# Optimization experiments

Hardware: AMD Instinct MI355X
Metric: run time of the kernel (lower is better)

Reference implementation:

```python
import jax, jax.numpy as jnp
import numpy as np

B, T, E, H, L = 16, 1024, 1024, 512, 6
C = 1024  # conv out channels


def _lstm_dir(x_tbi, Wih, Whh, bih, bhh):
    # x_tbi: [T, B, I]; single-direction LSTM, PyTorch gate order (i, f, g, o)
    Bn = x_tbi.shape[1]
    Hh = Whh.shape[1]
    b = bih + bhh
    def step(carry, xt):
        h, c = carry
        g = xt @ Wih.T + h @ Whh.T + b  # [B, 4H]
        i, f, gg, o = jnp.split(g, 4, axis=-1)
        c = jax.nn.sigmoid(f) * c + jax.nn.sigmoid(i) * jnp.tanh(gg)
        h = jax.nn.sigmoid(o) * jnp.tanh(c)
        return (h, c), h
    h0 = jnp.zeros((Bn, Hh), x_tbi.dtype)
    _, hs = jax.lax.scan(step, (h0, h0), x_tbi)
    return hs  # [T, B, H]


def _forward(embeddings, attention_mask, labels, conv_w, conv_b, bn_gamma, bn_beta,
             bn_mean, bn_var, lstm_Wih, lstm_Whh, lstm_bih, lstm_bhh,
             cls_w, cls_b, crf_start, crf_end, crf_trans):
    # Conv1d(E->1024, k=5, pad=2) on [B, C, T]
    x = jax.lax.conv_general_dilated(
        embeddings.astype(jnp.float32).transpose(0, 2, 1), conv_w,
        window_strides=(1,), padding=[(2, 2)],
        dimension_numbers=("NCH", "OIH", "NCH")) + conv_b[None, :, None]
    # BatchNorm1d (eval: running stats) fused + ReLU
    scale = bn_gamma / jnp.sqrt(bn_var + 1e-5)
    x = jax.nn.relu(x * scale[None, :, None] + (bn_beta - bn_mean * scale)[None, :, None])
    # time-major for the LSTM scans: [T, B, 1024]
    x = x.transpose(2, 0, 1)
    for l in range(3):
        fw = _lstm_dir(x, lstm_Wih[l, 0], lstm_Whh[l, 0], lstm_bih[l, 0], lstm_bhh[l, 0])
        bw = _lstm_dir(x[::-1], lstm_Wih[l, 1], lstm_Whh[l, 1], lstm_bih[l, 1], lstm_bhh[l, 1])[::-1]
        x = jnp.concatenate([fw, bw], axis=-1)  # [T, B, 2H]
    logits = x @ cls_w.T + cls_b  # [T, B, L]; dropout is identity in eval
    # CRF negative log-likelihood (torchcrf, batch_first handled by time-major layout)
    mask = (attention_mask.astype(bool) & (labels != -100)).T  # [T, B]
    tags = jnp.where(labels == -100, 0, labels).astype(jnp.int32).T  # [T, B]
    mf = mask.astype(logits.dtype)
    bidx = jnp.arange(logits.shape[1])
    # numerator: score of the given tag sequence
    score0 = crf_start[tags[0]] + logits[0, bidx, tags[0]]
    def num_step(carry, inp):
        score, prev = carry
        et, mt, mtf, tt = inp
        s = crf_trans[prev, tt] + et[bidx, tt]
        return (score + mtf * s, jnp.where(mt, tt, prev)), None
    (num, last), _ = jax.lax.scan(
        num_step, (score0, tags[0]), (logits[1:], mask[1:], mf[1:], tags[1:]))
    num = num + crf_end[last]
    # denominator: forward algorithm (log partition)
    def den_step(alpha, inp):
        et, mt = inp
        nxt = jax.nn.logsumexp(alpha[:, :, None] + crf_trans[None, :, :] + et[:, None, :], axis=1)
        return jnp.where(mt[:, None], nxt, alpha), None
    alpha, _ = jax.lax.scan(den_step, crf_start + logits[0], (logits[1:], mask[1:]))
    den = jax.nn.logsumexp(alpha + crf_end, axis=-1)
    return -(num - den).mean()  # reduction='mean' over batch, negated


def setup_inputs() -> dict:
    key = jax.random.key(0)
    ks = jax.random.split(key, 16)
    p = lambda k, shp: jax.random.normal(k, shp, jnp.float32) * 0.05
    return {
        "embeddings": jax.random.normal(ks[0], (B, T, E), jnp.float32),
        "attention_mask": jnp.ones((B, T), jnp.int32),
        "labels": jax.random.randint(ks[1], (B, T), 0, L, jnp.int32),
        "conv_w": p(ks[2], (C, E, 5)),
        "conv_b": p(ks[3], (C,)),
        "bn_gamma": jnp.ones((C,), jnp.float32),
        "bn_beta": jnp.zeros((C,), jnp.float32),
        "bn_mean": p(ks[4], (C,)),
        "bn_var": jax.random.uniform(ks[5], (C,), jnp.float32, 0.5, 1.5),
        "lstm_Wih": p(ks[6], (3, 2, 4 * H, C)),
        "lstm_Whh": p(ks[7], (3, 2, 4 * H, H)),
        "lstm_bih": p(ks[8], (3, 2, 4 * H)),
        "lstm_bhh": p(ks[9], (3, 2, 4 * H)),
        "cls_w": p(ks[10], (L, 2 * H)),
        "cls_b": p(ks[11], (L,)),
        "crf_start": p(ks[12], (L,)),
        "crf_end": p(ks[13], (L,)),
        "crf_trans": p(ks[14], (L, L)),
    }


def reference(embeddings, attention_mask, labels, conv_w, conv_b, bn_gamma, bn_beta,
              bn_mean, bn_var, lstm_Wih, lstm_Whh, lstm_bih, lstm_bhh,
              cls_w, cls_b, crf_start, crf_end, crf_trans):
    return _forward(embeddings, attention_mask, labels, conv_w, conv_b, bn_gamma,
                    bn_beta, bn_mean, bn_var, lstm_Wih, lstm_Whh, lstm_bih,
                    lstm_bhh, cls_w, cls_b, crf_start, crf_end, crf_trans)
```

## Files before the change

kernel.cpp:

```cpp
#include <hip/hip_runtime.h>


typedef short bf16_t;
typedef __attribute__((ext_vector_type(8))) short bf16x8;
typedef __attribute__((ext_vector_type(4))) float f32x4;

__device__ __forceinline__ bf16_t f2b(float x) {
  unsigned u = __float_as_uint(x);
  unsigned r = (u + 0x7fffu + ((u >> 16) & 1u)) >> 16;
  return (bf16_t)(unsigned short)r;
}
__device__ __forceinline__ float blo(unsigned u) { return __uint_as_float(u << 16); }
__device__ __forceinline__ float bhi(unsigned u) { return __uint_as_float(u & 0xffff0000u); }


__global__ void embed_pad_k(const float* __restrict__ E, bf16_t* __restrict__ P) {
  size_t i4 = ((size_t)blockIdx.x * 256 + threadIdx.x) * 4;
  if (i4 >= 16ul * 1028 * 1024) return;
  int e = (int)(i4 & 1023);
  size_t rest = i4 >> 10;
  int tp = (int)(rest % 1028);
  int b  = (int)(rest / 1028);
  bf16_t o[4];
  if (tp >= 2 && tp < 1026) {
    const float4 v = *(const float4*)(E + (((size_t)b * 1024 + (tp - 2)) * 1024 + e));
    o[0] = f2b(v.x); o[1] = f2b(v.y); o[2] = f2b(v.z); o[3] = f2b(v.w);
  } else {
    o[0] = o[1] = o[2] = o[3] = 0;
  }
  *(uint2*)(P + i4) = *(const uint2*)o;
}

__global__ void convw_cvt_k(const float* __restrict__ S, bf16_t* __restrict__ D) {
  int idx = blockIdx.x * 256 + threadIdx.x;
  if (idx >= 1024 * 1024) return;
  int c = idx >> 10, e = idx & 1023;
  const float* s = S + (size_t)idx * 5;
#pragma unroll
  for (int kk = 0; kk < 5; kk++) D[(size_t)c * 5120 + kk * 1024 + e] = f2b(s[kk]);
}

__global__ void bnfold_k(const float* cb, const float* g, const float* be,
                         const float* mn, const float* vr, float* a, float* dd) {
  int c = blockIdx.x * 256 + threadIdx.x;
  if (c < 1024) {
    float s = g[c] * rsqrtf(vr[c] + 1e-5f);
    a[c] = s;
    dd[c] = (cb[c] - mn[c]) * s + be[c];
  }
}

__global__ void wihcvt_k(const float* __restrict__ S, bf16_t* __restrict__ D) {
  size_t i = ((size_t)blockIdx.x * 256 + threadIdx.x) * 4;
  if (i >= 3ul * 2 * 2048 * 1024) return;
  float4 v = *(const float4*)(S + i);
  bf16_t o[4] = {f2b(v.x), f2b(v.y), f2b(v.z), f2b(v.w)};
  *(uint2*)(D + i) = *(const uint2*)o;
}

__global__ __launch_bounds__(256, 1) void gemm_bt(
    const bf16_t* __restrict__ A, const bf16_t* __restrict__ W,
    const float* __restrict__ bias0, const float* __restrict__ bias1,
    bf16_t* __restrict__ C, int M, int N, int K) {
  const int tid = threadIdx.x;
  const int nb = N >> 7;
  const int m0 = (blockIdx.x / nb) * 128, n0 = (blockIdx.x % nb) * 128;
  __shared__ bf16_t As[128][72];
  __shared__ bf16_t Bs[128][72];
  const int wv = tid >> 6, ln = tid & 63;
  const int wm = (wv >> 1) * 64, wn = (wv & 1) * 64;
  const int lb = ln & 15, lq = ln >> 4;
  f32x4 acc[4][4] = {};
  for (int k0 = 0; k0 < K; k0 += 64) {
    __syncthreads();
#pragma unroll
    for (int i = 0; i < 4; i++) {
      int idx = tid + i * 256, r = idx >> 3, ch = idx & 7;
      *(uint4*)&As[r][ch * 8] = *(const uint4*)(A + (size_t)(m0 + r) * K + k0 + ch * 8);
      *(uint4*)&Bs[r][ch * 8] = *(const uint4*)(W + (size_t)(n0 + r) * K + k0 + ch * 8);
    }
    __syncthreads();
#pragma unroll
    for (int kk = 0; kk < 2; kk++) {
      bf16x8 af[4], bfr[4];
#pragma unroll
      for (int t = 0; t < 4; t++) {
        af[t]  = *(const bf16x8*)&As[wm + t * 16 + lb][kk * 32 + lq * 8];
        bfr[t] = *(const bf16x8*)&Bs[wn + t * 16 + lb][kk * 32 + lq * 8];
      }
#pragma unroll
      for (int mt = 0; mt < 4; mt++)
#pragma unroll
        for (int nt = 0; nt < 4; nt++)
          acc[mt][nt] = __builtin_amdgcn_mfma_f32_16x16x32_bf16(af[mt], bfr[nt], acc[mt][nt], 0, 0, 0);
    }
  }
#pragma unroll
  for (int mt = 0; mt < 4; mt++)
#pragma unroll
    for (int nt = 0; nt < 4; nt++) {
      int col = n0 + wn + nt * 16 + lb;
      float bs = bias0[col] + bias1[col];
#pragma unroll
      for (int r = 0; r < 4; r++) {
        int row = m0 + wm + mt * 16 + lq * 4 + r;
        C[(size_t)row * N + col] = f2b(acc[mt][nt][r] + bs);
      }
    }
}

__global__ __launch_bounds__(256, 1) void conv_gemm(
    const bf16_t* __restrict__ EP, const bf16_t* __restrict__ Wc,
    const float* __restrict__ bn_a, const float* __restrict__ bn_d,
    bf16_t* __restrict__ X) {
  const int tid = threadIdx.x;
  const int m0 = (blockIdx.x >> 3) * 128, n0 = (blockIdx.x & 7) * 128;
  __shared__ bf16_t As[128][72];
  __shared__ bf16_t Bs[128][72];
  const int wv = tid >> 6, ln = tid & 63;
  const int wm = (wv >> 1) * 64, wn = (wv & 1) * 64;
  const int lb = ln & 15, lq = ln >> 4;
  f32x4 acc[4][4] = {};
  for (int kk = 0; kk < 5; kk++) {
    for (int k0 = 0; k0 < 1024; k0 += 64) {
      __syncthreads();
#pragma unroll
      for (int i = 0; i < 4; i++) {
        int idx = tid + i * 256, r = idx >> 3, ch = idx & 7;
        int m = m0 + r;
        const bf16_t* ap = EP + ((size_t)((m & 15) * 1028 + (m >> 4) + kk)) * 1024 + k0 + ch * 8;
        *(uint4*)&As[r][ch * 8] = *(const uint4*)ap;
        *(uint4*)&Bs[r][ch * 8] = *(const uint4*)(Wc + (size_t)(n0 + r) * 5120 + kk * 1024 + k0 + ch * 8);
      }
      __syncthreads();
#pragma unroll
      for (int kq = 0; kq < 2; kq++) {
        bf16x8 af[4], bfr[4];
#pragma unroll
        for (int t = 0; t < 4; t++) {
          af[t]  = *(const bf16x8*)&As[wm + t * 16 + lb][kq * 32 + lq * 8];
          bfr[t] = *(const bf16x8*)&Bs[wn + t * 16 + lb][kq * 32 + lq * 8];
        }
#pragma unroll
        for (int mt = 0; mt < 4; mt++)
#pragma unroll
          for (int nt = 0; nt < 4; nt++)
            acc[mt][nt] = __builtin_amdgcn_mfma_f32_16x16x32_bf16(af[mt], bfr[nt], acc[mt][nt], 0, 0, 0);
      }
    }
  }
#pragma unroll
  for (int mt = 0; mt < 4; mt++)
#pragma unroll
    for (int nt = 0; nt < 4; nt++) {
      int col = n0 + wn + nt * 16 + lb;
      float sa = bn_a[col], sd = bn_d[col];
#pragma unroll
      for (int r = 0; r < 4; r++) {
        int row = m0 + wm + mt * 16 + lq * 4 + r;
        float v = fmaxf(acc[mt][nt][r] * sa + sd, 0.f);
        X[(size_t)row * 1024 + col] = f2b(v);
      }
    }
}

__global__ __launch_bounds__(256, 1) void rec_kernel(
    const float* __restrict__ Whh,
    const bf16_t* __restrict__ gfw,
    const bf16_t* __restrict__ gbw,
    bf16_t* __restrict__ xout,
    bf16_t* __restrict__ hst,
    float* __restrict__ cst,
    unsigned* __restrict__ bar,
    int t0f, int t0b, int nsteps) {
  const int tid = threadIdx.x;
  const int d  = blockIdx.x >> 5;
  const int j0 = (blockIdx.x & 31) << 4;
  const int wv = tid >> 6;
  const int ln = tid & 63;
  const int lb = ln & 15;
  const int lq = ln >> 4;

  __shared__ bf16_t Hb[16][520];
  __shared__ float  Ex[4][16][17];

  bf16x8 afrag[16];
  {
    const float* wrow = Whh + ((size_t)(d * 2048 + wv * 512 + j0 + lb)) * 512;
#pragma unroll
    for (int kk = 0; kk < 16; kk++) {
      const float* wp = wrow + kk * 32 + lq * 8;
      float4 va = *(const float4*)wp;
      float4 vb = *(const float4*)(wp + 4);
      bf16x8 fr;
      fr[0] = f2b(va.x); fr[1] = f2b(va.y); fr[2] = f2b(va.z); fr[3] = f2b(va.w);
      fr[4] = f2b(vb.x); fr[5] = f2b(vb.y); fr[6] = f2b(vb.z); fr[7] = f2b(vb.w);
      afrag[kk] = fr;
    }
  }
  const int cb = tid >> 4;
  const int cj = tid & 15;
  float creg = cst[((size_t)d * 16 + cb) * 512 + j0 + cj];
  const bf16_t* gates = (d == 0) ? gfw : gbw;

  unsigned g0, g1;
  {
    const int trow = (d == 0) ? 0 : (nsteps - 1);
    const unsigned* gp = (const unsigned*)(gates + ((size_t)trow * 16 + lb) * 2048 + wv * 512 + j0 + lq * 4);
    g0 = gp[0]; g1 = gp[1];
  }

  for (int s = 0; s < nsteps; s++) {
    const int rb = (s & 1) ^ 1, wb = s & 1;
    if (s > 0) {
      if (tid == 0) {
        unsigned target = (unsigned)(64 * s);
        while (__hip_atomic_load(bar, __ATOMIC_RELAXED, __HIP_MEMORY_SCOPE_AGENT) < target)
          __builtin_amdgcn_s_sleep(1);
      }
      __syncthreads();
    }
    {
      const unsigned long long* hsrc =
          (const unsigned long long*)(hst + ((size_t)rb * 2 + d) * 16 * 512);
      unsigned long long v[8];
#pragma unroll
      for (int i = 0; i < 8; i++)
        v[i] = __hip_atomic_load(hsrc + tid + i * 256, __ATOMIC_RELAXED, __HIP_MEMORY_SCOPE_AGENT);
#pragma unroll
      for (int i = 0; i < 8; i++) {
        int idx = tid + i * 256;
        *(unsigned long long*)&Hb[idx >> 7][(idx & 127) * 4] = v[i];
      }
    }
    __syncthreads();
    const int t = (d == 0) ? (t0f + s) : (t0b + nsteps - 1 - s);
    f32x4 acc;
    acc[0] = blo(g0); acc[1] = bhi(g0); acc[2] = blo(g1); acc[3] = bhi(g1);
#pragma unroll
    for (int kk = 0; kk < 16; kk++) {
      bf16x8 bfr = *(const bf16x8*)&Hb[lb][kk * 32 + lq * 8];
      acc = __builtin_amdgcn_mfma_f32_16x16x32_bf16(afrag[kk], bfr, acc, 0, 0, 0);
    }
    if (s + 1 < nsteps) {
      const int trn = (d == 0) ? (s + 1) : (nsteps - 2 - s);
      const unsigned* gpn = (const unsigned*)(gates + ((size_t)trn * 16 + lb) * 2048 + wv * 512 + j0 + lq * 4);
      g0 = gpn[0]; g1 = gpn[1];
    }
#pragma unroll
    for (int r = 0; r < 4; r++) Ex[wv][lq * 4 + r][lb] = acc[r];
    __syncthreads();
    float gi = Ex[0][cj][cb], gf = Ex[1][cj][cb], gg = Ex[2][cj][cb], go = Ex[3][cj][cb];
    float si = 1.f / (1.f + expf(-gi));
    float sf = 1.f / (1.f + expf(-gf));
    float so = 1.f / (1.f + expf(-go));
    creg = sf * creg + si * tanhf(gg);
    float h = so * tanhf(creg);
    bf16_t hb = f2b(h);
    {
      int hi = __shfl_down((int)(unsigned)(unsigned short)hb, 1, 64);
      if ((cj & 1) == 0) {
        unsigned val = (unsigned)(unsigned short)hb | ((unsigned)hi << 16);
        unsigned* hp = (unsigned*)(hst + (((size_t)wb * 2 + d) * 16 + cb) * 512 + j0 + cj);
        __hip_atomic_store(hp, val, __ATOMIC_RELAXED, __HIP_MEMORY_SCOPE_AGENT);
      }
    }
    xout[((size_t)t * 16 + cb) * 1024 + d * 512 + j0 + cj] = hb;
    asm volatile("s_waitcnt vmcnt(0)" ::: "memory");
    __syncthreads();
    if (tid == 0)
      __hip_atomic_fetch_add(bar, 1u, __ATOMIC_RELAXED, __HIP_MEMORY_SCOPE_AGENT);
  }
  cst[((size_t)d * 16 + cb) * 512 + j0 + cj] = creg;
}

__global__ void cls_kernel(const bf16_t* __restrict__ X, const float* __restrict__ Wc,
                           const float* __restrict__ bc, float* __restrict__ Lg) {
  int wv = threadIdx.x >> 6, ln = threadIdx.x & 63;
  size_t m = (size_t)blockIdx.x * 4 + wv;
  const bf16_t* xr = X + m * 1024 + ln * 16;
  uint4 v0 = *(const uint4*)xr;
  uint4 v1 = *(const uint4*)(xr + 8);
  float xv[16];
  const unsigned* p0 = (const unsigned*)&v0;
  const unsigned* p1 = (const unsigned*)&v1;
#pragma unroll
  for (int i = 0; i < 4; i++) { xv[2 * i] = blo(p0[i]); xv[2 * i + 1] = bhi(p0[i]); }
#pragma unroll
  for (int i = 0; i < 4; i++) { xv[8 + 2 * i] = blo(p1[i]); xv[8 + 2 * i + 1] = bhi(p1[i]); }
#pragma unroll
  for (int l = 0; l < 6; l++) {
    const float* wr = Wc + l * 1024 + ln * 16;
    float p = 0.f;
#pragma unroll
    for (int i = 0; i < 16; i++) p += xv[i] * wr[i];
#pragma unroll
    for (int off = 32; off; off >>= 1) p += __shfl_xor(p, off, 64);
    if (ln == 0) Lg[m * 6 + l] = p + bc[l];
  }
}

__global__ void crf_kernel(const float* __restrict__ Lg, const int* __restrict__ attn,
                           const int* __restrict__ labels, const float* __restrict__ start,
                           const float* __restrict__ endw, const float* __restrict__ trans,
                           float* __restrict__ out) {
  int b = blockIdx.x, ln = threadIdx.x;
  __shared__ float str[36];
  __shared__ int tg[1024];
  __shared__ unsigned char mk[1024];
  if (ln < 36) str[ln] = trans[ln];
  for (int t = ln; t < 1024; t += 64) {
    int lab = labels[b * 1024 + t];
    mk[t] = (unsigned char)((attn[b * 1024 + t] != 0) && (lab != -100));
    tg[t] = (lab == -100) ? 0 : lab;
  }
  __syncthreads();
  int j = ln;
  bool act = j < 6;
  float alpha = act ? (start[j] + Lg[(size_t)b * 6 + j]) : -1e30f;
  for (int t = 1; t < 1024; t++) {
    float vv[6], mx = -1e30f;
#pragma unroll
    for (int i = 0; i < 6; i++) {
      float ai = __shfl(alpha, i, 64);
      float v = ai + str[i * 6 + (act ? j : 0)];
      vv[i] = v;
      mx = fmaxf(mx, v);
    }
    float sm = 0.f;
#pragma unroll
    for (int i = 0; i < 6; i++) sm += expf(vv[i] - mx);
    float na = mx + logf(sm) + (act ? Lg[((size_t)t * 16 + b) * 6 + j] : 0.f);
    if (mk[t] && act) alpha = na;
  }
  float z = act ? (alpha + endw[j]) : -1e30f;
  float zm = z;
#pragma unroll
  for (int i = 0; i < 6; i++) zm = fmaxf(zm, __shfl(z, i, 64));
  float zs = act ? expf(z - zm) : 0.f;
  float tot = 0.f;
#pragma unroll
  for (int i = 0; i < 6; i++) tot += __shfl(zs, i, 64);
  float den = zm + logf(tot);
  if (ln == 0) {
    float score = start[tg[0]] + Lg[(size_t)b * 6 + tg[0]];
    int prev = tg[0];
    for (int t = 1; t < 1024; t++) {
      if (mk[t]) {
        score += str[prev * 6 + tg[t]] + Lg[((size_t)t * 16 + b) * 6 + tg[t]];
        prev = tg[t];
      }
    }
    score += endw[prev];
    atomicAdd(out, (den - score) * (1.0f / 16.0f));
  }
}

extern "C" void kernel_launch(void* const* d_in, const int* in_sizes, int n_in,
                              void* d_out, int out_size, void* d_ws, size_t ws_size,
                              hipStream_t stream) {
  const float* emb    = (const float*)d_in[0];
  const int*   attn   = (const int*)d_in[1];
  const int*   labels = (const int*)d_in[2];
  const float* convw  = (const float*)d_in[3];
  const float* convb  = (const float*)d_in[4];
  const float* bng    = (const float*)d_in[5];
  const float* bnb    = (const float*)d_in[6];
  const float* bnm    = (const float*)d_in[7];
  const float* bnv    = (const float*)d_in[8];
  const float* wih    = (const float*)d_in[9];
  const float* whh    = (const float*)d_in[10];
  const float* bih    = (const float*)d_in[11];
  const float* bhh    = (const float*)d_in[12];
  const float* clsw   = (const float*)d_in[13];
  const float* clsb   = (const float*)d_in[14];
  const float* crfs   = (const float*)d_in[15];
  const float* crfe   = (const float*)d_in[16];
  const float* crft   = (const float*)d_in[17];
  (void)in_sizes; (void)n_in; (void)out_size; (void)ws_size;

  char* w = (char*)d_ws;
  auto alloc = [&](size_t bytes) { char* p = w; w += (bytes + 255) & ~(size_t)255; return p; };
  bf16_t* emb_pad = (bf16_t*)alloc(16ul * 1028 * 1024 * 2);
  bf16_t* wconv   = (bf16_t*)alloc(1024ul * 5120 * 2);
  float*  bn_a    = (float*)alloc(4096);
  float*  bn_d    = (float*)alloc(4096);
  bf16_t* wihb    = (bf16_t*)alloc(3ul * 2 * 2048 * 1024 * 2);
  bf16_t* xA      = (bf16_t*)alloc(16384ul * 1024 * 2);
  bf16_t* xB      = (bf16_t*)alloc(16384ul * 1024 * 2);
  bf16_t* gfw     = (bf16_t*)alloc(8192ul * 2048 * 2);
  bf16_t* gbw     = (bf16_t*)alloc(8192ul * 2048 * 2);
  bf16_t* hst     = (bf16_t*)alloc(2ul * 2 * 16 * 512 * 2);
  float*  cst     = (float*)alloc(2ul * 16 * 512 * 4);
  float*  lgt     = (float*)alloc(16384ul * 6 * 4);
  unsigned* bar   = (unsigned*)alloc(256);

  hipMemsetAsync(d_out, 0, 4, stream);

  embed_pad_k<<<16448, 256, 0, stream>>>(emb, emb_pad);
  convw_cvt_k<<<4096, 256, 0, stream>>>(convw, wconv);
  bnfold_k<<<4, 256, 0, stream>>>(convb, bng, bnb, bnm, bnv, bn_a, bn_d);
  wihcvt_k<<<12288, 256, 0, stream>>>(wih, wihb);

  conv_gemm<<<128 * 8, 256, 0, stream>>>(emb_pad, wconv, bn_a, bn_d, xA);

  bf16_t* xin = xA;
  bf16_t* xout = xB;
  for (int l = 0; l < 3; l++) {
    hipMemsetAsync(hst, 0, 2ul * 2 * 16 * 512 * 2, stream);
    hipMemsetAsync(cst, 0, 2ul * 16 * 512 * 4, stream);
    for (int c = 0; c < 2; c++) {
      int t0f = c * 512, t0b = (1 - c) * 512;
      gemm_bt<<<64 * 16, 256, 0, stream>>>(
          xin + (size_t)t0f * 16 * 1024, wihb + ((size_t)l * 2 + 0) * 2048 * 1024,
          bih + (l * 2 + 0) * 2048, bhh + (l * 2 + 0) * 2048, gfw, 8192, 2048, 1024);
      gemm_bt<<<64 * 16, 256, 0, stream>>>(
          xin + (size_t)t0b * 16 * 1024, wihb + ((size_t)l * 2 + 1) * 2048 * 1024,
          bih + (l * 2 + 1) * 2048, bhh + (l * 2 + 1) * 2048, gbw, 8192, 2048, 1024);
      hipMemsetAsync(bar, 0, 4, stream);
      rec_kernel<<<64, 256, 0, stream>>>(whh + (size_t)l * 2 * 2048 * 512,
                                         gfw, gbw, xout, hst, cst, bar, t0f, t0b, 512);
    }
    bf16_t* tmp = xin; xin = xout; xout = tmp;
  }

  cls_kernel<<<4096, 256, 0, stream>>>(xin, clsw, clsb, lgt);
  crf_kernel<<<16, 64, 0, stream>>>(lgt, attn, labels, crfs, crfe, crft, (float*)d_out);
}
```

Baseline: 11.05 ms.

## Replace global step barrier with tag-stamped hidden-state words in recurrent LSTM kernel

The persistent recurrence kernel no longer uses a shared atomic counter barrier. Each packed pair of hidden values is now stored as a 64-bit word carrying a step tag. Consumer warps spin on their own slice of the state until every tag matches the expected step, then unpack the data into shared memory. This removes the per-step fetch-add, the vmcnt drain, the single-thread spin and an extra block-wide sync. It also splits the MFMA accumulation into two independent chains to shorten the dependency latency. The cost is doubled state-buffer traffic and repeated polling reads of the full slice.

After: 9.208 ms. 16.7% less time.

```diff
diff --git a/kernel.cpp b/kernel.cpp
--- a/kernel.cpp
+++ b/kernel.cpp
@@ -169,10 +169,9 @@
     const bf16_t* __restrict__ gfw,
     const bf16_t* __restrict__ gbw,
     bf16_t* __restrict__ xout,
-    bf16_t* __restrict__ hst,
+    unsigned long long* __restrict__ hstT,
     float* __restrict__ cst,
-    unsigned* __restrict__ bar,
-    int t0f, int t0b, int nsteps) {
+    int t0f, int t0b, int nsteps, int tag_base) {
   const int tid = threadIdx.x;
   const int d  = blockIdx.x >> 5;
   const int j0 = (blockIdx.x & 31) << 4;
@@ -212,35 +211,37 @@
 
   for (int s = 0; s < nsteps; s++) {
     const int rb = (s & 1) ^ 1, wb = s & 1;
-    if (s > 0) {
-      if (tid == 0) {
-        unsigned target = (unsigned)(64 * s);
-        while (__hip_atomic_load(bar, __ATOMIC_RELAXED, __HIP_MEMORY_SCOPE_AGENT) < target)
-          __builtin_amdgcn_s_sleep(1);
-      }
-      __syncthreads();
-    }
     {
-      const unsigned long long* hsrc =
-          (const unsigned long long*)(hst + ((size_t)rb * 2 + d) * 16 * 512);
-      unsigned long long v[8];
-#pragma unroll
-      for (int i = 0; i < 8; i++)
-        v[i] = __hip_atomic_load(hsrc + tid + i * 256, __ATOMIC_RELAXED, __HIP_MEMORY_SCOPE_AGENT);
-#pragma unroll
-      for (int i = 0; i < 8; i++) {
-        int idx = tid + i * 256;
-        *(unsigned long long*)&Hb[idx >> 7][(idx & 127) * 4] = v[i];
+      const unsigned long long* src =
+          hstT + (((size_t)rb * 2 + d) * 16 + (wv << 2)) * 256;
+      const unsigned expect = (unsigned)(tag_base + s);
+      unsigned long long v[16];
+      bool ok;
+      do {
+        ok = true;
+#pragma unroll
+        for (int i = 0; i < 16; i++)
+          v[i] = __hip_atomic_load(src + i * 64 + ln, __ATOMIC_RELAXED, __HIP_MEMORY_SCOPE_AGENT);
+#pragma unroll
+        for (int i = 0; i < 16; i++) ok = ok && ((unsigned)(v[i] >> 32) == expect);
+      } while (!__all(ok));
+#pragma unroll
+      for (int i = 0; i < 16; i++) {
+        int idx = i * 64 + ln;
+        *(unsigned*)&Hb[(wv << 2) + (idx >> 8)][(idx & 255) * 2] = (unsigned)v[i];
       }
     }
     __syncthreads();
     const int t = (d == 0) ? (t0f + s) : (t0b + nsteps - 1 - s);
-    f32x4 acc;
-    acc[0] = blo(g0); acc[1] = bhi(g0); acc[2] = blo(g1); acc[3] = bhi(g1);
-#pragma unroll
-    for (int kk = 0; kk < 16; kk++) {
-      bf16x8 bfr = *(const bf16x8*)&Hb[lb][kk * 32 + lq * 8];
-      acc = __builtin_amdgcn_mfma_f32_16x16x32_bf16(afrag[kk], bfr, acc, 0, 0, 0);
+    f32x4 acc0, acc1;
+    acc0[0] = blo(g0); acc0[1] = bhi(g0); acc0[2] = blo(g1); acc0[3] = bhi(g1);
+    acc1[0] = 0.f; acc1[1] = 0.f; acc1[2] = 0.f; acc1[3] = 0.f;
+#pragma unroll
+    for (int kk = 0; kk < 8; kk++) {
+      bf16x8 b0 = *(const bf16x8*)&Hb[lb][(2 * kk) * 32 + lq * 8];
+      bf16x8 b1 = *(const bf16x8*)&Hb[lb][(2 * kk + 1) * 32 + lq * 8];
+      acc0 = __builtin_amdgcn_mfma_f32_16x16x32_bf16(afrag[2 * kk], b0, acc0, 0, 0, 0);
+      acc1 = __builtin_amdgcn_mfma_f32_16x16x32_bf16(afrag[2 * kk + 1], b1, acc1, 0, 0, 0);
     }
     if (s + 1 < nsteps) {
       const int trn = (d == 0) ? (s + 1) : (nsteps - 2 - s);
@@ -248,7 +249,7 @@
       g0 = gpn[0]; g1 = gpn[1];
     }
 #pragma unroll
-    for (int r = 0; r < 4; r++) Ex[wv][lq * 4 + r][lb] = acc[r];
+    for (int r = 0; r < 4; r++) Ex[wv][lq * 4 + r][lb] = acc0[r] + acc1[r];
     __syncthreads();
     float gi = Ex[0][cj][cb], gf = Ex[1][cj][cb], gg = Ex[2][cj][cb], go = Ex[3][cj][cb];
     float si = 1.f / (1.f + expf(-gi));
@@ -260,16 +261,15 @@
     {
       int hi = __shfl_down((int)(unsigned)(unsigned short)hb, 1, 64);
       if ((cj & 1) == 0) {
-        unsigned val = (unsigned)(unsigned short)hb | ((unsigned)hi << 16);
-        unsigned* hp = (unsigned*)(hst + (((size_t)wb * 2 + d) * 16 + cb) * 512 + j0 + cj);
+        unsigned data = (unsigned)(unsigned short)hb | ((unsigned)hi << 16);
+        unsigned long long val =
+            ((unsigned long long)(unsigned)(tag_base + s + 1) << 32) | data;
+        unsigned long long* hp =
+            hstT + (((size_t)wb * 2 + d) * 16 + cb) * 256 + ((j0 + cj) >> 1);
         __hip_atomic_store(hp, val, __ATOMIC_RELAXED, __HIP_MEMORY_SCOPE_AGENT);
       }
     }
     xout[((size_t)t * 16 + cb) * 1024 + d * 512 + j0 + cj] = hb;
-    asm volatile("s_waitcnt vmcnt(0)" ::: "memory");
-    __syncthreads();
-    if (tid == 0)
-      __hip_atomic_fetch_add(bar, 1u, __ATOMIC_RELAXED, __HIP_MEMORY_SCOPE_AGENT);
   }
   cst[((size_t)d * 16 + cb) * 512 + j0 + cj] = creg;
 }
@@ -390,10 +390,9 @@
   bf16_t* xB      = (bf16_t*)alloc(16384ul * 1024 * 2);
   bf16_t* gfw     = (bf16_t*)alloc(8192ul * 2048 * 2);
   bf16_t* gbw     = (bf16_t*)alloc(8192ul * 2048 * 2);
-  bf16_t* hst     = (bf16_t*)alloc(2ul * 2 * 16 * 512 * 2);
+  unsigned long long* hstT = (unsigned long long*)alloc(2ul * 2 * 16 * 256 * 8);
   float*  cst     = (float*)alloc(2ul * 16 * 512 * 4);
   float*  lgt     = (float*)alloc(16384ul * 6 * 4);
-  unsigned* bar   = (unsigned*)alloc(256);
 
   hipMemsetAsync(d_out, 0, 4, stream);
 
@@ -407,7 +406,7 @@
   bf16_t* xin = xA;
   bf16_t* xout = xB;
   for (int l = 0; l < 3; l++) {
-    hipMemsetAsync(hst, 0, 2ul * 2 * 16 * 512 * 2, stream);
+    hipMemsetAsync(hstT, 0, 2ul * 2 * 16 * 256 * 8, stream);
     hipMemsetAsync(cst, 0, 2ul * 16 * 512 * 4, stream);
     for (int c = 0; c < 2; c++) {
       int t0f = c * 512, t0b = (1 - c) * 512;
@@ -417,9 +416,8 @@
       gemm_bt<<<64 * 16, 256, 0, stream>>>(
           xin + (size_t)t0b * 16 * 1024, wihb + ((size_t)l * 2 + 1) * 2048 * 1024,
           bih + (l * 2 + 1) * 2048, bhh + (l * 2 + 1) * 2048, gbw, 8192, 2048, 1024);
-      hipMemsetAsync(bar, 0, 4, stream);
       rec_kernel<<<64, 256, 0, stream>>>(whh + (size_t)l * 2 * 2048 * 512,
-                                         gfw, gbw, xout, hst, cst, bar, t0f, t0b, 512);
+                                         gfw, gbw, xout, hstT, cst, t0f, t0b, 512, c * 512);
     }
     bf16_t* tmp = xin; xin = xout; xout = tmp;
   }
```
